# Kernel tuning notes

Measured on AMD Instinct MI355X. Metric: run time of the kernel, lower is better.

## Reference

```python
import jax, jax.numpy as jnp
import numpy as np

NEG_INF = jnp.finfo(jnp.float32).min

def setup_inputs() -> dict:
    key = jax.random.key(0)
    k1, k2, k3, k4 = jax.random.split(key, 4)
    B, H, S, DK, DV = 2, 16, 2048, 64, 64
    Q = jax.random.normal(k1, (B, H, S, DK), dtype=jnp.float32)
    K = jax.random.normal(k2, (B, H, S, DK), dtype=jnp.float32)
    V = jax.random.normal(k3, (B, H, S, DV), dtype=jnp.float32)
    mask = jax.random.randint(k4, (B, 1, S, S), 0, 2, dtype=jnp.int32)
    return {"Q": Q, "K": K, "V": V, "mask": mask}

def reference(Q, K, V, mask):
    d_k = Q.shape[-1]
    # scores: [B, H, Sq, Sk]
    scores = jnp.einsum('bhqd,bhkd->bhqk', Q, K) / jnp.sqrt(jnp.float32(d_k))
    scores = jnp.where(mask == 0, NEG_INF, scores)
    attn_weights = jax.nn.softmax(scores, axis=-1)
    # dropout p=0.0 -> identity (eval-mode reference)
    output = jnp.einsum('bhqk,bhkv->bhqv', attn_weights, V)
    return (output, attn_weights)
```

## Files before the change

kernel.cpp:

```cpp
#include <hip/hip_runtime.h>


typedef __attribute__((ext_vector_type(4))) float f32x4;
typedef __attribute__((ext_vector_type(8))) short s16x8;
typedef __attribute__((ext_vector_type(4))) unsigned short u16x4;
typedef __attribute__((ext_vector_type(8))) unsigned short u16x8;
typedef __attribute__((ext_vector_type(4))) unsigned int u32x4;

#define S_LEN 2048
#define D_DIM 64
#define H_NUM 16
#define B_NUM 2
#define NT    32
#define SW    32
#define QSCALE 0.18033688011112042f

__device__ __forceinline__ int swz(int row, int colByte) {
  return row * 128 + (colByte ^ ((row & 7) << 4));
}

__device__ __forceinline__ unsigned short f2bf(float f) {
  unsigned int x = __builtin_bit_cast(unsigned int, f);
  x = (x + 0x7FFFu + ((x >> 16) & 1u)) >> 16;
  return (unsigned short)x;
}

__device__ __forceinline__ unsigned cvt_pk_bf16(float lo, float hi) {
  unsigned r;
  asm("v_cvt_pk_bf16_f32 %0, %1, %2" : "=v"(r) : "v"(lo), "v"(hi));
  return r;
}

__device__ __forceinline__ f32x4 mfma16(f32x4 acc, s16x8 a, s16x8 b) {
  return __builtin_amdgcn_mfma_f32_16x16x32_bf16(a, b, acc, 0, 0, 0);
}


__global__ __launch_bounds__(256) void prep_kernel(
    const float* __restrict__ Q, const float* __restrict__ K,
    const float* __restrict__ V, const int* __restrict__ m,
    u16x4* __restrict__ Q16, u16x4* __restrict__ K16,
    unsigned short* __restrict__ VT, unsigned long long* __restrict__ bits)
{
  const int blk = blockIdx.x;
  const int tid = threadIdx.x;

  if (blk < 1024) {
    __shared__ unsigned short t[64][72];
    const int bh = blk >> 5;
    const int st = blk & 31;
    const float* src = V + ((size_t)bh * S_LEN + st * 64) * D_DIM;
    const int r0 = tid >> 4;
    const int c  = (tid & 15) * 4;
#pragma unroll
    for (int i = 0; i < 4; ++i) {
      const int r = r0 + i * 16;
      float4 v = *(const float4*)(src + r * D_DIM + c);
      t[c + 0][r] = f2bf(v.x); t[c + 1][r] = f2bf(v.y);
      t[c + 2][r] = f2bf(v.z); t[c + 3][r] = f2bf(v.w);
    }
    __syncthreads();
#pragma unroll
    for (int i = 0; i < 4; ++i) {
      const int idx = tid + i * 256;
      const int d  = idx >> 4;
      const int t0 = (idx & 15) * 4;
      const int sp = ((t0 >> 5) & 1) * 32 + ((t0 & 7) >> 2) * 16 + ((t0 >> 3) & 3) * 4;
      u16x4 o = *(const u16x4*)&t[d][sp];
      *(u16x4*)(VT + ((size_t)bh * D_DIM + d) * S_LEN + st * 64 + t0) = o;
    }
  } else if (blk < 2048) {
    const int n4 = B_NUM * H_NUM * S_LEN * D_DIM / 4;
    const int step = 1024 * 256;
    for (int i = (blk - 1024) * 256 + tid; i < n4; i += step) {
      float4 q = ((const float4*)Q)[i];
      Q16[i] = u16x4{f2bf(q.x * QSCALE), f2bf(q.y * QSCALE),
                     f2bf(q.z * QSCALE), f2bf(q.w * QSCALE)};
      float4 k = ((const float4*)K)[i];
      K16[i] = u16x4{f2bf(k.x), f2bf(k.y), f2bf(k.z), f2bf(k.w)};
    }
  } else {
    const int total = B_NUM * S_LEN * S_LEN;
    const int step  = 1024 * 256;
    for (int i = (blk - 2048) * 256 + tid; i < total; i += step) {
      unsigned long long b = __ballot(m[i] != 0);
      if ((tid & 63) == 0) bits[i >> 6] = b;
    }
  }
}


__global__ __launch_bounds__(256) void attn_fused_kernel(
    const unsigned short* __restrict__ Q16, const unsigned short* __restrict__ K16,
    const unsigned short* __restrict__ VT16, const unsigned long long* __restrict__ Mb,
    float* __restrict__ Op, float* __restrict__ Wp)
{
  const int tid  = threadIdx.x;
  const int lane = tid & 63;
  const int wv   = tid >> 6;
  const int l15  = lane & 15;
  const int g4   = lane >> 4;

  const int wg = blockIdx.x;
  const int lg = (wg & 7) * 128 + (wg >> 3);
  const int qt = lg & 31;
  const int bh = lg >> 5;
  const int b  = bh >> 4;

  __shared__ __align__(16) char lds[32768];
  char* Kbuf = lds;
  char* Vbuf = lds + 16384;

  const unsigned short* Qg16 = Q16 + ((size_t)bh * S_LEN + qt * 64 + wv * 16 + l15) * D_DIM + g4 * 8;
  const unsigned short* Kg16 = K16 + (size_t)bh * S_LEN * D_DIM;
  const unsigned short* Vg   = VT16 + (size_t)bh * D_DIM * S_LEN;
  float* Og = Op + ((size_t)bh * S_LEN + qt * 64) * D_DIM;
  float* Wg = Wp + ((size_t)bh * S_LEN + qt * 64) * S_LEN;
  const unsigned long long* Mg = Mb + ((size_t)b * S_LEN + qt * 64) * SW;

  const s16x8 qa0 = *(const s16x8*)Qg16;
  const s16x8 qa1 = *(const s16x8*)(Qg16 + 32);

  f32x4 oacc[4];
#pragma unroll
  for (int i = 0; i < 4; ++i) oacc[i] = f32x4{0.f, 0.f, 0.f, 0.f};
  float lps = 0.f;

  const int sr  = tid >> 3;
  const int ss  = tid & 7;
  const int ssb = ss * 16;

  {
    u16x8 k0 = *(const u16x8*)(Kg16 + (size_t)sr * D_DIM + ss * 8);
    u16x8 k1 = *(const u16x8*)(Kg16 + (size_t)(sr + 32) * D_DIM + ss * 8);
    u16x8 v0 = *(const u16x8*)(Vg + (size_t)sr * S_LEN + ss * 8);
    u16x8 v1 = *(const u16x8*)(Vg + (size_t)(sr + 32) * S_LEN + ss * 8);
    *(u16x8*)(Kbuf + swz(sr, ssb))      = k0;
    *(u16x8*)(Kbuf + swz(sr + 32, ssb)) = k1;
    *(u16x8*)(Vbuf + swz(sr, ssb))      = v0;
    *(u16x8*)(Vbuf + swz(sr + 32, ssb)) = v1;
  }
  __syncthreads();

  int cur = 0;
  for (int kt = 0; kt < NT; ++kt) {
    const int ktn = (kt + 1 < NT) ? kt + 1 : kt;
    u16x8 kr0 = *(const u16x8*)(Kg16 + (size_t)(ktn * 64 + sr) * D_DIM + ss * 8);
    u16x8 kr1 = *(const u16x8*)(Kg16 + (size_t)(ktn * 64 + sr + 32) * D_DIM + ss * 8);
    u16x8 vr0 = *(const u16x8*)(Vg + (size_t)sr * S_LEN + ktn * 64 + ss * 8);
    u16x8 vr1 = *(const u16x8*)(Vg + (size_t)(sr + 32) * S_LEN + ktn * 64 + ss * 8);
    __builtin_amdgcn_sched_barrier(0);

    char* Kc = Kbuf + cur * 8192;
    char* Vc = Vbuf + cur * 8192;

    const unsigned long long mw = Mg[(wv * 16 + l15) * SW + kt];

    f32x4 sacc[4];
#pragma unroll
    for (int i = 0; i < 4; ++i) sacc[i] = f32x4{0.f, 0.f, 0.f, 0.f};
#pragma unroll
    for (int ct = 0; ct < 4; ++ct) {
      s16x8 b0 = *(const s16x8*)(Kc + swz(ct * 16 + l15, g4 * 16));
      s16x8 b1 = *(const s16x8*)(Kc + swz(ct * 16 + l15, g4 * 16 + 64));
      sacc[ct] = mfma16(sacc[ct], b0, qa0);
      sacc[ct] = mfma16(sacc[ct], b1, qa1);
    }

    float ev[4][4];
#pragma unroll
    for (int ct = 0; ct < 4; ++ct) {
#pragma unroll
      for (int r = 0; r < 4; ++r) {
        float e = __builtin_amdgcn_exp2f(sacc[ct][r]);
        e = ((mw >> (ct * 16 + g4 * 4 + r)) & 1ull) ? e : 0.f;
        ev[ct][r] = e;
      }
      lps += (ev[ct][0] + ev[ct][1]) + (ev[ct][2] + ev[ct][3]);
    }
    const u32x4 a0 = {cvt_pk_bf16(ev[0][0], ev[0][1]), cvt_pk_bf16(ev[0][2], ev[0][3]),
                      cvt_pk_bf16(ev[1][0], ev[1][1]), cvt_pk_bf16(ev[1][2], ev[1][3])};
    const u32x4 a1 = {cvt_pk_bf16(ev[2][0], ev[2][1]), cvt_pk_bf16(ev[2][2], ev[2][3]),
                      cvt_pk_bf16(ev[3][0], ev[3][1]), cvt_pk_bf16(ev[3][2], ev[3][3])};
    const s16x8 pa0 = __builtin_bit_cast(s16x8, a0);
    const s16x8 pa1 = __builtin_bit_cast(s16x8, a1);

#pragma unroll
    for (int ct = 0; ct < 4; ++ct) {
      s16x8 v0 = *(const s16x8*)(Vc + swz(ct * 16 + l15, g4 * 16));
      s16x8 v1 = *(const s16x8*)(Vc + swz(ct * 16 + l15, g4 * 16 + 64));
      oacc[ct] = mfma16(oacc[ct], pa0, v0);
      oacc[ct] = mfma16(oacc[ct], pa1, v1);
    }

    char* Kn = Kbuf + (cur ^ 1) * 8192;
    char* Vn = Vbuf + (cur ^ 1) * 8192;
    *(u16x8*)(Kn + swz(sr, ssb))      = kr0;
    *(u16x8*)(Kn + swz(sr + 32, ssb)) = kr1;
    *(u16x8*)(Vn + swz(sr, ssb))      = vr0;
    *(u16x8*)(Vn + swz(sr + 32, ssb)) = vr1;
    __syncthreads();
    cur ^= 1;
  }

  lps += __shfl_xor(lps, 16);
  lps += __shfl_xor(lps, 32);
  const float lpr = 1.0f / lps;

  float lpn[4];
#pragma unroll
  for (int r = 0; r < 4; ++r) lpn[r] = __shfl(lpr, g4 * 4 + r);

#pragma unroll
  for (int ct = 0; ct < 4; ++ct)
#pragma unroll
    for (int r = 0; r < 4; ++r)
      Og[(size_t)(wv * 16 + g4 * 4 + r) * D_DIM + ct * 16 + l15] = oacc[ct][r] * lpn[r];

  __builtin_amdgcn_sched_barrier(0);

  float* Wrow = Wg + (size_t)(wv * 16 + l15) * S_LEN;
  const unsigned long long* Mrow = Mg + (wv * 16 + l15) * SW;

  s16x8 kb0[4], kb1[4];
#pragma unroll
  for (int ct = 0; ct < 4; ++ct) {
    const unsigned short* kp = Kg16 + (size_t)(ct * 16 + l15) * D_DIM + g4 * 8;
    kb0[ct] = *(const s16x8*)kp;
    kb1[ct] = *(const s16x8*)(kp + 32);
  }

  for (int kt = 0; kt < NT; ++kt) {
    const int ktn = (kt < NT - 1) ? kt + 1 : kt;
    s16x8 nk0[4], nk1[4];
#pragma unroll
    for (int ct = 0; ct < 4; ++ct) {
      const unsigned short* kp = Kg16 + (size_t)(ktn * 64 + ct * 16 + l15) * D_DIM + g4 * 8;
      nk0[ct] = *(const s16x8*)kp;
      nk1[ct] = *(const s16x8*)(kp + 32);
    }

    const unsigned long long mw = Mrow[kt];

    f32x4 sacc[4];
#pragma unroll
    for (int i = 0; i < 4; ++i) sacc[i] = f32x4{0.f, 0.f, 0.f, 0.f};
#pragma unroll
    for (int ct = 0; ct < 4; ++ct) {
      sacc[ct] = mfma16(sacc[ct], kb0[ct], qa0);
      sacc[ct] = mfma16(sacc[ct], kb1[ct], qa1);
    }

#pragma unroll
    for (int ct = 0; ct < 4; ++ct) {
      f32x4 w;
#pragma unroll
      for (int r = 0; r < 4; ++r) {
        float e = __builtin_amdgcn_exp2f(sacc[ct][r]);
        w[r] = ((mw >> (ct * 16 + g4 * 4 + r)) & 1ull) ? e * lpr : 0.f;
      }
      __builtin_nontemporal_store(w,
          (f32x4*)(Wrow + (size_t)kt * 64 + ct * 16 + g4 * 4));
    }
#pragma unroll
    for (int ct = 0; ct < 4; ++ct) { kb0[ct] = nk0[ct]; kb1[ct] = nk1[ct]; }
  }
}


__global__ __launch_bounds__(256) void attn_fwd_kernel(
    const float* __restrict__ Qp, const float* __restrict__ Kp, const float* __restrict__ Vp,
    const int* __restrict__ Mi, float* __restrict__ Op, float* __restrict__ Wp)
{
  const int tid  = threadIdx.x;
  const int lane = tid & 63;
  const int wv   = tid >> 6;
  const int l15  = lane & 15;
  const int g4   = lane >> 4;

  const int wg = blockIdx.x;
  const int lg = (wg & 7) * 128 + (wg >> 3);
  const int qt = lg & 31;
  const int bh = lg >> 5;
  const int b  = bh >> 4;

  __shared__ __align__(16) char lds[32768];
  char* Qs  = lds;
  char* Ks  = lds + 8192;
  char* VTs = lds + 16384;
  char* Ps  = lds + 24576 + (wv << 11);

  const float* Qg = Qp + ((size_t)bh * S_LEN + qt * 64) * D_DIM;
  const float* Kg = Kp + (size_t)bh * S_LEN * D_DIM;
  const float* Vg = Vp + (size_t)bh * S_LEN * D_DIM;
  float* Og = Op + ((size_t)bh * S_LEN + qt * 64) * D_DIM;
  float* Wg = Wp + ((size_t)bh * S_LEN + qt * 64) * S_LEN;
  const int* Mig = Mi + ((size_t)b * S_LEN + qt * 64) * S_LEN;

  {
    const int r0 = tid >> 4;
    const int c  = (tid & 15) * 4;
#pragma unroll
    for (int i = 0; i < 4; ++i) {
      const int r = r0 + i * 16;
      float4 v = *(const float4*)(Qg + r * D_DIM + c);
      ushort4 p; p.x = f2bf(v.x); p.y = f2bf(v.y); p.z = f2bf(v.z); p.w = f2bf(v.w);
      *(ushort4*)(Qs + swz(r, c * 2)) = p;
    }
  }
  __syncthreads();
  const s16x8 qa0 = *(const s16x8*)(Qs + swz(wv * 16 + l15, g4 * 16));
  const s16x8 qa1 = *(const s16x8*)(Qs + swz(wv * 16 + l15, g4 * 16 + 64));

  f32x4 oacc[4];
#pragma unroll
  for (int i = 0; i < 4; ++i) oacc[i] = f32x4{0.f, 0.f, 0.f, 0.f};
  float lp[4] = {0.f, 0.f, 0.f, 0.f};

  const int qrow = wv * 16 + g4 * 4;

  for (int kt = 0; kt < NT; ++kt) {
    __syncthreads();
    {
      const int r0 = tid >> 4;
      const int c  = (tid & 15) * 4;
      const float* Kt = Kg + kt * 64 * D_DIM;
#pragma unroll
      for (int i = 0; i < 4; ++i) {
        const int r = r0 + i * 16;
        float4 v = *(const float4*)(Kt + r * D_DIM + c);
        ushort4 p; p.x = f2bf(v.x); p.y = f2bf(v.y); p.z = f2bf(v.z); p.w = f2bf(v.w);
        *(ushort4*)(Ks + swz(r, c * 2)) = p;
      }
      const float* Vt = Vg + kt * 64 * D_DIM;
#pragma unroll
      for (int i = 0; i < 2; ++i) {
        const int rr = (tid >> 4) * 2 + i * 32;
        float4 a  = *(const float4*)(Vt + rr * D_DIM + c);
        float4 bq = *(const float4*)(Vt + (rr + 1) * D_DIM + c);
        const float av[4] = {a.x, a.y, a.z, a.w};
        const float bv[4] = {bq.x, bq.y, bq.z, bq.w};
#pragma unroll
        for (int j = 0; j < 4; ++j) {
          unsigned pk = (unsigned)f2bf(av[j]) | ((unsigned)f2bf(bv[j]) << 16);
          *(unsigned*)(VTs + swz(c + j, rr * 2)) = pk;
        }
      }
    }
    __syncthreads();

    f32x4 sacc[4];
#pragma unroll
    for (int i = 0; i < 4; ++i) sacc[i] = f32x4{0.f, 0.f, 0.f, 0.f};
#pragma unroll
    for (int ct = 0; ct < 4; ++ct) {
      s16x8 b0 = *(const s16x8*)(Ks + swz(ct * 16 + l15, g4 * 16));
      s16x8 b1 = *(const s16x8*)(Ks + swz(ct * 16 + l15, g4 * 16 + 64));
      sacc[ct] = mfma16(sacc[ct], qa0, b0);
      sacc[ct] = mfma16(sacc[ct], qa1, b1);
    }

#pragma unroll
    for (int ct = 0; ct < 4; ++ct) {
#pragma unroll
      for (int r = 0; r < 4; ++r) {
        float e = __expf(sacc[ct][r] * 0.125f);
        bool keep = Mig[(size_t)(qrow + r) * S_LEN + kt * 64 + ct * 16 + l15] != 0;
        e = keep ? e : 0.f;
        lp[r] += e;
        *(unsigned short*)(Ps + swz(g4 * 4 + r, (ct * 16 + l15) * 2)) = f2bf(e);
      }
    }
    asm volatile("s_waitcnt lgkmcnt(0)" ::: "memory");
    __builtin_amdgcn_sched_barrier(0);

    const s16x8 pa0 = *(const s16x8*)(Ps + swz(l15, g4 * 16));
    const s16x8 pa1 = *(const s16x8*)(Ps + swz(l15, g4 * 16 + 64));
#pragma unroll
    for (int ct = 0; ct < 4; ++ct) {
      s16x8 v0 = *(const s16x8*)(VTs + swz(ct * 16 + l15, g4 * 16));
      s16x8 v1 = *(const s16x8*)(VTs + swz(ct * 16 + l15, g4 * 16 + 64));
      oacc[ct] = mfma16(oacc[ct], pa0, v0);
      oacc[ct] = mfma16(oacc[ct], pa1, v1);
    }
  }

#pragma unroll
  for (int r = 0; r < 4; ++r) {
    float v = lp[r];
    v += __shfl_xor(v, 1);
    v += __shfl_xor(v, 2);
    v += __shfl_xor(v, 4);
    v += __shfl_xor(v, 8);
    lp[r] = 1.0f / v;
  }

#pragma unroll
  for (int ct = 0; ct < 4; ++ct)
#pragma unroll
    for (int r = 0; r < 4; ++r)
      Og[(size_t)(qrow + r) * D_DIM + ct * 16 + l15] = oacc[ct][r] * lp[r];

  for (int kt = 0; kt < NT; ++kt) {
    __syncthreads();
    {
      const int r0 = tid >> 4;
      const int c  = (tid & 15) * 4;
      const float* Kt = Kg + kt * 64 * D_DIM;
#pragma unroll
      for (int i = 0; i < 4; ++i) {
        const int r = r0 + i * 16;
        float4 v = *(const float4*)(Kt + r * D_DIM + c);
        ushort4 p; p.x = f2bf(v.x); p.y = f2bf(v.y); p.z = f2bf(v.z); p.w = f2bf(v.w);
        *(ushort4*)(Ks + swz(r, c * 2)) = p;
      }
    }
    __syncthreads();

    f32x4 sacc[4];
#pragma unroll
    for (int i = 0; i < 4; ++i) sacc[i] = f32x4{0.f, 0.f, 0.f, 0.f};
#pragma unroll
    for (int ct = 0; ct < 4; ++ct) {
      s16x8 b0 = *(const s16x8*)(Ks + swz(ct * 16 + l15, g4 * 16));
      s16x8 b1 = *(const s16x8*)(Ks + swz(ct * 16 + l15, g4 * 16 + 64));
      sacc[ct] = mfma16(sacc[ct], qa0, b0);
      sacc[ct] = mfma16(sacc[ct], qa1, b1);
    }

#pragma unroll
    for (int ct = 0; ct < 4; ++ct) {
#pragma unroll
      for (int r = 0; r < 4; ++r) {
        float e = __expf(sacc[ct][r] * 0.125f);
        bool keep = Mig[(size_t)(qrow + r) * S_LEN + kt * 64 + ct * 16 + l15] != 0;
        e = keep ? e : 0.f;
        __builtin_nontemporal_store(e * lp[r],
            Wg + (size_t)(qrow + r) * S_LEN + kt * 64 + ct * 16 + l15);
      }
    }
  }
}

extern "C" void kernel_launch(void* const* d_in, const int* in_sizes, int n_in,
                              void* d_out, int out_size, void* d_ws, size_t ws_size,
                              hipStream_t stream) {
  (void)in_sizes; (void)n_in; (void)out_size;
  const float* Q   = (const float*)d_in[0];
  const float* K   = (const float*)d_in[1];
  const float* V   = (const float*)d_in[2];
  const int* mask  = (const int*)d_in[3];
  float* Out = (float*)d_out;
  float* W   = Out + (size_t)B_NUM * H_NUM * S_LEN * D_DIM;

  const size_t bits_bytes = (size_t)(B_NUM * S_LEN * S_LEN / 64) * 8;
  const size_t t16_bytes  = (size_t)B_NUM * H_NUM * S_LEN * D_DIM * 2;
  unsigned long long* bits = (unsigned long long*)d_ws;

  if (ws_size >= bits_bytes + 3 * t16_bytes) {
    unsigned short* Q16 = (unsigned short*)((char*)d_ws + bits_bytes);
    unsigned short* K16 = Q16 + t16_bytes / 2;
    unsigned short* VT  = K16 + t16_bytes / 2;
    prep_kernel<<<3072, 256, 0, stream>>>(Q, K, V, mask,
                                          (u16x4*)Q16, (u16x4*)K16, VT, bits);
    attn_fused_kernel<<<1024, 256, 0, stream>>>(Q16, K16, VT, bits, Out, W);
  } else {
    attn_fwd_kernel<<<1024, 256, 0, stream>>>(Q, K, V, mask, Out, W);
  }
}
```

Before: 239.9 us.

## Share K/V LDS tiles across two query tiles with 512-thread blocks

```diff
diff --git a/kernel.cpp b/kernel.cpp
--- a/kernel.cpp
+++ b/kernel.cpp
@@ -90,7 +90,7 @@
 }
 
 
-__global__ __launch_bounds__(256) void attn_fused_kernel(
+__global__ __launch_bounds__(512, 4) void attn_fused_kernel(
     const unsigned short* __restrict__ Q16, const unsigned short* __restrict__ K16,
     const unsigned short* __restrict__ VT16, const unsigned long long* __restrict__ Mb,
     float* __restrict__ Op, float* __restrict__ Wp)
@@ -100,18 +100,20 @@
   const int wv   = tid >> 6;
   const int l15  = lane & 15;
   const int g4   = lane >> 4;
+  const int wt   = wv & 3;
 
   const int wg = blockIdx.x;
-  const int lg = (wg & 7) * 128 + (wg >> 3);
-  const int qt = lg & 31;
-  const int bh = lg >> 5;
+  const int lg = (wg & 7) * 64 + (wg >> 3);
+  const int tp = lg & 15;
+  const int bh = lg >> 4;
   const int b  = bh >> 4;
+  const int qt = tp * 2 + (wv >> 2);
 
   __shared__ __align__(16) char lds[32768];
   char* Kbuf = lds;
   char* Vbuf = lds + 16384;
 
-  const unsigned short* Qg16 = Q16 + ((size_t)bh * S_LEN + qt * 64 + wv * 16 + l15) * D_DIM + g4 * 8;
+  const unsigned short* Qg16 = Q16 + ((size_t)bh * S_LEN + qt * 64 + wt * 16 + l15) * D_DIM + g4 * 8;
   const unsigned short* Kg16 = K16 + (size_t)bh * S_LEN * D_DIM;
   const unsigned short* Vg   = VT16 + (size_t)bh * D_DIM * S_LEN;
   float* Og = Op + ((size_t)bh * S_LEN + qt * 64) * D_DIM;
@@ -132,29 +134,23 @@
 
   {
     u16x8 k0 = *(const u16x8*)(Kg16 + (size_t)sr * D_DIM + ss * 8);
-    u16x8 k1 = *(const u16x8*)(Kg16 + (size_t)(sr + 32) * D_DIM + ss * 8);
     u16x8 v0 = *(const u16x8*)(Vg + (size_t)sr * S_LEN + ss * 8);
-    u16x8 v1 = *(const u16x8*)(Vg + (size_t)(sr + 32) * S_LEN + ss * 8);
-    *(u16x8*)(Kbuf + swz(sr, ssb))      = k0;
-    *(u16x8*)(Kbuf + swz(sr + 32, ssb)) = k1;
-    *(u16x8*)(Vbuf + swz(sr, ssb))      = v0;
-    *(u16x8*)(Vbuf + swz(sr + 32, ssb)) = v1;
+    *(u16x8*)(Kbuf + swz(sr, ssb)) = k0;
+    *(u16x8*)(Vbuf + swz(sr, ssb)) = v0;
   }
   __syncthreads();
 
   int cur = 0;
   for (int kt = 0; kt < NT; ++kt) {
     const int ktn = (kt + 1 < NT) ? kt + 1 : kt;
-    u16x8 kr0 = *(const u16x8*)(Kg16 + (size_t)(ktn * 64 + sr) * D_DIM + ss * 8);
-    u16x8 kr1 = *(const u16x8*)(Kg16 + (size_t)(ktn * 64 + sr + 32) * D_DIM + ss * 8);
-    u16x8 vr0 = *(const u16x8*)(Vg + (size_t)sr * S_LEN + ktn * 64 + ss * 8);
-    u16x8 vr1 = *(const u16x8*)(Vg + (size_t)(sr + 32) * S_LEN + ktn * 64 + ss * 8);
+    u16x8 kr = *(const u16x8*)(Kg16 + (size_t)(ktn * 64 + sr) * D_DIM + ss * 8);
+    u16x8 vr = *(const u16x8*)(Vg + (size_t)sr * S_LEN + ktn * 64 + ss * 8);
     __builtin_amdgcn_sched_barrier(0);
 
     char* Kc = Kbuf + cur * 8192;
     char* Vc = Vbuf + cur * 8192;
 
-    const unsigned long long mw = Mg[(wv * 16 + l15) * SW + kt];
+    const unsigned long long mw = Mg[(wt * 16 + l15) * SW + kt];
 
     f32x4 sacc[4];
 #pragma unroll
@@ -167,23 +163,23 @@
       sacc[ct] = mfma16(sacc[ct], b1, qa1);
     }
 
-    float ev[4][4];
-#pragma unroll
-    for (int ct = 0; ct < 4; ++ct) {
-#pragma unroll
-      for (int r = 0; r < 4; ++r) {
-        float e = __builtin_amdgcn_exp2f(sacc[ct][r]);
-        e = ((mw >> (ct * 16 + g4 * 4 + r)) & 1ull) ? e : 0.f;
-        ev[ct][r] = e;
-      }
-      lps += (ev[ct][0] + ev[ct][1]) + (ev[ct][2] + ev[ct][3]);
-    }
-    const u32x4 a0 = {cvt_pk_bf16(ev[0][0], ev[0][1]), cvt_pk_bf16(ev[0][2], ev[0][3]),
-                      cvt_pk_bf16(ev[1][0], ev[1][1]), cvt_pk_bf16(ev[1][2], ev[1][3])};
-    const u32x4 a1 = {cvt_pk_bf16(ev[2][0], ev[2][1]), cvt_pk_bf16(ev[2][2], ev[2][3]),
-                      cvt_pk_bf16(ev[3][0], ev[3][1]), cvt_pk_bf16(ev[3][2], ev[3][3])};
-    const s16x8 pa0 = __builtin_bit_cast(s16x8, a0);
-    const s16x8 pa1 = __builtin_bit_cast(s16x8, a1);
+    unsigned pw[8];
+#pragma unroll
+    for (int ct = 0; ct < 4; ++ct) {
+      float e0 = __builtin_amdgcn_exp2f(sacc[ct][0]);
+      float e1 = __builtin_amdgcn_exp2f(sacc[ct][1]);
+      float e2 = __builtin_amdgcn_exp2f(sacc[ct][2]);
+      float e3 = __builtin_amdgcn_exp2f(sacc[ct][3]);
+      e0 = ((mw >> (ct * 16 + g4 * 4 + 0)) & 1ull) ? e0 : 0.f;
+      e1 = ((mw >> (ct * 16 + g4 * 4 + 1)) & 1ull) ? e1 : 0.f;
+      e2 = ((mw >> (ct * 16 + g4 * 4 + 2)) & 1ull) ? e2 : 0.f;
+      e3 = ((mw >> (ct * 16 + g4 * 4 + 3)) & 1ull) ? e3 : 0.f;
+      lps += (e0 + e1) + (e2 + e3);
+      pw[2 * ct]     = cvt_pk_bf16(e0, e1);
+      pw[2 * ct + 1] = cvt_pk_bf16(e2, e3);
+    }
+    const s16x8 pa0 = __builtin_bit_cast(s16x8, u32x4{pw[0], pw[1], pw[2], pw[3]});
+    const s16x8 pa1 = __builtin_bit_cast(s16x8, u32x4{pw[4], pw[5], pw[6], pw[7]});
 
 #pragma unroll
     for (int ct = 0; ct < 4; ++ct) {
@@ -195,10 +191,8 @@
 
     char* Kn = Kbuf + (cur ^ 1) * 8192;
     char* Vn = Vbuf + (cur ^ 1) * 8192;
-    *(u16x8*)(Kn + swz(sr, ssb))      = kr0;
-    *(u16x8*)(Kn + swz(sr + 32, ssb)) = kr1;
-    *(u16x8*)(Vn + swz(sr, ssb))      = vr0;
-    *(u16x8*)(Vn + swz(sr + 32, ssb)) = vr1;
+    *(u16x8*)(Kn + swz(sr, ssb)) = kr;
+    *(u16x8*)(Vn + swz(sr, ssb)) = vr;
     __syncthreads();
     cur ^= 1;
   }
@@ -215,12 +209,12 @@
   for (int ct = 0; ct < 4; ++ct)
 #pragma unroll
     for (int r = 0; r < 4; ++r)
-      Og[(size_t)(wv * 16 + g4 * 4 + r) * D_DIM + ct * 16 + l15] = oacc[ct][r] * lpn[r];
+      Og[(size_t)(wt * 16 + g4 * 4 + r) * D_DIM + ct * 16 + l15] = oacc[ct][r] * lpn[r];
 
   __builtin_amdgcn_sched_barrier(0);
 
-  float* Wrow = Wg + (size_t)(wv * 16 + l15) * S_LEN;
-  const unsigned long long* Mrow = Mg + (wv * 16 + l15) * SW;
+  float* Wrow = Wg + (size_t)(wt * 16 + l15) * S_LEN;
+  const unsigned long long* Mrow = Mg + (wt * 16 + l15) * SW;
 
   s16x8 kb0[4], kb1[4];
 #pragma unroll
@@ -463,7 +457,7 @@
     unsigned short* VT  = K16 + t16_bytes / 2;
     prep_kernel<<<3072, 256, 0, stream>>>(Q, K, V, mask,
                                           (u16x4*)Q16, (u16x4*)K16, VT, bits);
-    attn_fused_kernel<<<1024, 256, 0, stream>>>(Q16, K16, VT, bits, Out, W);
+    attn_fused_kernel<<<512, 512, 0, stream>>>(Q16, K16, VT, bits, Out, W);
   } else {
     attn_fwd_kernel<<<1024, 256, 0, stream>>>(Q, K, V, mask, Out, W);
   }
```

Measured after the change: 230.1 us. 1.04x faster.

## Split attention into row-sum pass and fused PV plus weights-write pass

Applied to the files above, without the earlier changes.

```diff
diff --git a/kernel.cpp b/kernel.cpp
--- a/kernel.cpp
+++ b/kernel.cpp
@@ -90,10 +90,9 @@
 }
 
 
-__global__ __launch_bounds__(256) void attn_fused_kernel(
+__global__ __launch_bounds__(256) void attn_rowsum_kernel(
     const unsigned short* __restrict__ Q16, const unsigned short* __restrict__ K16,
-    const unsigned short* __restrict__ VT16, const unsigned long long* __restrict__ Mb,
-    float* __restrict__ Op, float* __restrict__ Wp)
+    const unsigned long long* __restrict__ Mb, float* __restrict__ lpq)
 {
   const int tid  = threadIdx.x;
   const int lane = tid & 63;
@@ -107,6 +106,90 @@
   const int bh = lg >> 5;
   const int b  = bh >> 4;
 
+  __shared__ __align__(16) char Kbuf[16384];
+
+  const unsigned short* Qg16 = Q16 + ((size_t)bh * S_LEN + qt * 64 + wv * 16 + l15) * D_DIM + g4 * 8;
+  const unsigned short* Kg16 = K16 + (size_t)bh * S_LEN * D_DIM;
+  float* lpg = lpq + (size_t)bh * S_LEN + qt * 64;
+  const unsigned long long* Mg = Mb + ((size_t)b * S_LEN + qt * 64) * SW;
+
+  const s16x8 qa0 = *(const s16x8*)Qg16;
+  const s16x8 qa1 = *(const s16x8*)(Qg16 + 32);
+
+  float lps = 0.f;
+
+  const int sr  = tid >> 3;
+  const int ss  = tid & 7;
+  const int ssb = ss * 16;
+
+  {
+    u16x8 k0 = *(const u16x8*)(Kg16 + (size_t)sr * D_DIM + ss * 8);
+    u16x8 k1 = *(const u16x8*)(Kg16 + (size_t)(sr + 32) * D_DIM + ss * 8);
+    *(u16x8*)(Kbuf + swz(sr, ssb))      = k0;
+    *(u16x8*)(Kbuf + swz(sr + 32, ssb)) = k1;
+  }
+  __syncthreads();
+
+  int cur = 0;
+  for (int kt = 0; kt < NT; ++kt) {
+    const int ktn = (kt + 1 < NT) ? kt + 1 : kt;
+    u16x8 kr0 = *(const u16x8*)(Kg16 + (size_t)(ktn * 64 + sr) * D_DIM + ss * 8);
+    u16x8 kr1 = *(const u16x8*)(Kg16 + (size_t)(ktn * 64 + sr + 32) * D_DIM + ss * 8);
+    __builtin_amdgcn_sched_barrier(0);
+
+    char* Kc = Kbuf + cur * 8192;
+    const unsigned long long mw = Mg[(wv * 16 + l15) * SW + kt];
+
+    f32x4 sacc[4];
+#pragma unroll
+    for (int i = 0; i < 4; ++i) sacc[i] = f32x4{0.f, 0.f, 0.f, 0.f};
+#pragma unroll
+    for (int ct = 0; ct < 4; ++ct) {
+      s16x8 b0 = *(const s16x8*)(Kc + swz(ct * 16 + l15, g4 * 16));
+      s16x8 b1 = *(const s16x8*)(Kc + swz(ct * 16 + l15, g4 * 16 + 64));
+      sacc[ct] = mfma16(sacc[ct], b0, qa0);
+      sacc[ct] = mfma16(sacc[ct], b1, qa1);
+    }
+
+#pragma unroll
+    for (int ct = 0; ct < 4; ++ct) {
+#pragma unroll
+      for (int r = 0; r < 4; ++r) {
+        float e = __builtin_amdgcn_exp2f(sacc[ct][r]);
+        lps += ((mw >> (ct * 16 + g4 * 4 + r)) & 1ull) ? e : 0.f;
+      }
+    }
+
+    char* Kn = Kbuf + (cur ^ 1) * 8192;
+    *(u16x8*)(Kn + swz(sr, ssb))      = kr0;
+    *(u16x8*)(Kn + swz(sr + 32, ssb)) = kr1;
+    __syncthreads();
+    cur ^= 1;
+  }
+
+  lps += __shfl_xor(lps, 16);
+  lps += __shfl_xor(lps, 32);
+  if (g4 == 0) lpg[wv * 16 + l15] = 1.0f / lps;
+}
+
+
+__global__ __launch_bounds__(256) void attn_main_kernel(
+    const unsigned short* __restrict__ Q16, const unsigned short* __restrict__ K16,
+    const unsigned short* __restrict__ VT16, const unsigned long long* __restrict__ Mb,
+    const float* __restrict__ lpq, float* __restrict__ Op, float* __restrict__ Wp)
+{
+  const int tid  = threadIdx.x;
+  const int lane = tid & 63;
+  const int wv   = tid >> 6;
+  const int l15  = lane & 15;
+  const int g4   = lane >> 4;
+
+  const int wg = blockIdx.x;
+  const int lg = (wg & 7) * 128 + (wg >> 3);
+  const int qt = lg & 31;
+  const int bh = lg >> 5;
+  const int b  = bh >> 4;
+
   __shared__ __align__(16) char lds[32768];
   char* Kbuf = lds;
   char* Vbuf = lds + 16384;
@@ -115,16 +198,21 @@
   const unsigned short* Kg16 = K16 + (size_t)bh * S_LEN * D_DIM;
   const unsigned short* Vg   = VT16 + (size_t)bh * D_DIM * S_LEN;
   float* Og = Op + ((size_t)bh * S_LEN + qt * 64) * D_DIM;
-  float* Wg = Wp + ((size_t)bh * S_LEN + qt * 64) * S_LEN;
+  float* Wrow = Wp + ((size_t)bh * S_LEN + qt * 64 + wv * 16 + l15) * S_LEN;
   const unsigned long long* Mg = Mb + ((size_t)b * S_LEN + qt * 64) * SW;
+  const float* lpg = lpq + (size_t)bh * S_LEN + qt * 64;
 
   const s16x8 qa0 = *(const s16x8*)Qg16;
   const s16x8 qa1 = *(const s16x8*)(Qg16 + 32);
 
+  const float lpr = lpg[wv * 16 + l15];
+  float lpn[4];
+#pragma unroll
+  for (int r = 0; r < 4; ++r) lpn[r] = lpg[wv * 16 + g4 * 4 + r];
+
   f32x4 oacc[4];
 #pragma unroll
   for (int i = 0; i < 4; ++i) oacc[i] = f32x4{0.f, 0.f, 0.f, 0.f};
-  float lps = 0.f;
 
   const int sr  = tid >> 3;
   const int ss  = tid & 7;
@@ -167,23 +255,25 @@
       sacc[ct] = mfma16(sacc[ct], b1, qa1);
     }
 
-    float ev[4][4];
-#pragma unroll
-    for (int ct = 0; ct < 4; ++ct) {
-#pragma unroll
-      for (int r = 0; r < 4; ++r) {
-        float e = __builtin_amdgcn_exp2f(sacc[ct][r]);
-        e = ((mw >> (ct * 16 + g4 * 4 + r)) & 1ull) ? e : 0.f;
-        ev[ct][r] = e;
-      }
-      lps += (ev[ct][0] + ev[ct][1]) + (ev[ct][2] + ev[ct][3]);
-    }
-    const u32x4 a0 = {cvt_pk_bf16(ev[0][0], ev[0][1]), cvt_pk_bf16(ev[0][2], ev[0][3]),
-                      cvt_pk_bf16(ev[1][0], ev[1][1]), cvt_pk_bf16(ev[1][2], ev[1][3])};
-    const u32x4 a1 = {cvt_pk_bf16(ev[2][0], ev[2][1]), cvt_pk_bf16(ev[2][2], ev[2][3]),
-                      cvt_pk_bf16(ev[3][0], ev[3][1]), cvt_pk_bf16(ev[3][2], ev[3][3])};
-    const s16x8 pa0 = __builtin_bit_cast(s16x8, a0);
-    const s16x8 pa1 = __builtin_bit_cast(s16x8, a1);
+    unsigned pw[8];
+#pragma unroll
+    for (int ct = 0; ct < 4; ++ct) {
+      float e0 = __builtin_amdgcn_exp2f(sacc[ct][0]);
+      float e1 = __builtin_amdgcn_exp2f(sacc[ct][1]);
+      float e2 = __builtin_amdgcn_exp2f(sacc[ct][2]);
+      float e3 = __builtin_amdgcn_exp2f(sacc[ct][3]);
+      e0 = ((mw >> (ct * 16 + g4 * 4 + 0)) & 1ull) ? e0 : 0.f;
+      e1 = ((mw >> (ct * 16 + g4 * 4 + 1)) & 1ull) ? e1 : 0.f;
+      e2 = ((mw >> (ct * 16 + g4 * 4 + 2)) & 1ull) ? e2 : 0.f;
+      e3 = ((mw >> (ct * 16 + g4 * 4 + 3)) & 1ull) ? e3 : 0.f;
+      f32x4 w = {e0 * lpr, e1 * lpr, e2 * lpr, e3 * lpr};
+      __builtin_nontemporal_store(w,
+          (f32x4*)(Wrow + (size_t)kt * 64 + ct * 16 + g4 * 4));
+      pw[2 * ct]     = cvt_pk_bf16(e0, e1);
+      pw[2 * ct + 1] = cvt_pk_bf16(e2, e3);
+    }
+    const s16x8 pa0 = __builtin_bit_cast(s16x8, u32x4{pw[0], pw[1], pw[2], pw[3]});
+    const s16x8 pa1 = __builtin_bit_cast(s16x8, u32x4{pw[4], pw[5], pw[6], pw[7]});
 
 #pragma unroll
     for (int ct = 0; ct < 4; ++ct) {
@@ -203,68 +293,11 @@
     cur ^= 1;
   }
 
-  lps += __shfl_xor(lps, 16);
-  lps += __shfl_xor(lps, 32);
-  const float lpr = 1.0f / lps;
-
-  float lpn[4];
-#pragma unroll
-  for (int r = 0; r < 4; ++r) lpn[r] = __shfl(lpr, g4 * 4 + r);
-
 #pragma unroll
   for (int ct = 0; ct < 4; ++ct)
 #pragma unroll
     for (int r = 0; r < 4; ++r)
       Og[(size_t)(wv * 16 + g4 * 4 + r) * D_DIM + ct * 16 + l15] = oacc[ct][r] * lpn[r];
-
-  __builtin_amdgcn_sched_barrier(0);
-
-  float* Wrow = Wg + (size_t)(wv * 16 + l15) * S_LEN;
-  const unsigned long long* Mrow = Mg + (wv * 16 + l15) * SW;
-
-  s16x8 kb0[4], kb1[4];
-#pragma unroll
-  for (int ct = 0; ct < 4; ++ct) {
-    const unsigned short* kp = Kg16 + (size_t)(ct * 16 + l15) * D_DIM + g4 * 8;
-    kb0[ct] = *(const s16x8*)kp;
-    kb1[ct] = *(const s16x8*)(kp + 32);
-  }
-
-  for (int kt = 0; kt < NT; ++kt) {
-    const int ktn = (kt < NT - 1) ? kt + 1 : kt;
-    s16x8 nk0[4], nk1[4];
-#pragma unroll
-    for (int ct = 0; ct < 4; ++ct) {
-      const unsigned short* kp = Kg16 + (size_t)(ktn * 64 + ct * 16 + l15) * D_DIM + g4 * 8;
-      nk0[ct] = *(const s16x8*)kp;
-      nk1[ct] = *(const s16x8*)(kp + 32);
-    }
-
-    const unsigned long long mw = Mrow[kt];
-
-    f32x4 sacc[4];
-#pragma unroll
-    for (int i = 0; i < 4; ++i) sacc[i] = f32x4{0.f, 0.f, 0.f, 0.f};
-#pragma unroll
-    for (int ct = 0; ct < 4; ++ct) {
-      sacc[ct] = mfma16(sacc[ct], kb0[ct], qa0);
-      sacc[ct] = mfma16(sacc[ct], kb1[ct], qa1);
-    }
-
-#pragma unroll
-    for (int ct = 0; ct < 4; ++ct) {
-      f32x4 w;
-#pragma unroll
-      for (int r = 0; r < 4; ++r) {
-        float e = __builtin_amdgcn_exp2f(sacc[ct][r]);
-        w[r] = ((mw >> (ct * 16 + g4 * 4 + r)) & 1ull) ? e * lpr : 0.f;
-      }
-      __builtin_nontemporal_store(w,
-          (f32x4*)(Wrow + (size_t)kt * 64 + ct * 16 + g4 * 4));
-    }
-#pragma unroll
-    for (int ct = 0; ct < 4; ++ct) { kb0[ct] = nk0[ct]; kb1[ct] = nk1[ct]; }
-  }
 }
 
 
@@ -455,15 +488,18 @@
 
   const size_t bits_bytes = (size_t)(B_NUM * S_LEN * S_LEN / 64) * 8;
   const size_t t16_bytes  = (size_t)B_NUM * H_NUM * S_LEN * D_DIM * 2;
+  const size_t lp_bytes   = (size_t)B_NUM * H_NUM * S_LEN * 4;
   unsigned long long* bits = (unsigned long long*)d_ws;
 
-  if (ws_size >= bits_bytes + 3 * t16_bytes) {
+  if (ws_size >= bits_bytes + 3 * t16_bytes + lp_bytes) {
     unsigned short* Q16 = (unsigned short*)((char*)d_ws + bits_bytes);
     unsigned short* K16 = Q16 + t16_bytes / 2;
     unsigned short* VT  = K16 + t16_bytes / 2;
+    float* lpq = (float*)((char*)d_ws + bits_bytes + 3 * t16_bytes);
     prep_kernel<<<3072, 256, 0, stream>>>(Q, K, V, mask,
                                           (u16x4*)Q16, (u16x4*)K16, VT, bits);
-    attn_fused_kernel<<<1024, 256, 0, stream>>>(Q16, K16, VT, bits, Out, W);
+    attn_rowsum_kernel<<<1024, 256, 0, stream>>>(Q16, K16, bits, lpq);
+    attn_main_kernel<<<1024, 256, 0, stream>>>(Q16, K16, VT, bits, lpq, Out, W);
   } else {
     attn_fwd_kernel<<<1024, 256, 0, stream>>>(Q, K, V, mask, Out, W);
   }
```

Result: faster. 230.2 us (median of 3 runs) (-4.1%).

## Precompute softmax row sums in separate kernel and write weights during PV pass

Applied to the files above, without the earlier changes.

```diff
diff --git a/kernel.cpp b/kernel.cpp
--- a/kernel.cpp
+++ b/kernel.cpp
@@ -13,6 +13,7 @@
 #define B_NUM 2
 #define NT    32
 #define SW    32
+#define BHS   (B_NUM * H_NUM * S_LEN)
 #define QSCALE 0.18033688011112042f
 
 __device__ __forceinline__ int swz(int row, int colByte) {
@@ -90,10 +91,9 @@
 }
 
 
-__global__ __launch_bounds__(256) void attn_fused_kernel(
+__global__ __launch_bounds__(256) void attn_rowsum_kernel(
     const unsigned short* __restrict__ Q16, const unsigned short* __restrict__ K16,
-    const unsigned short* __restrict__ VT16, const unsigned long long* __restrict__ Mb,
-    float* __restrict__ Op, float* __restrict__ Wp)
+    const unsigned long long* __restrict__ Mb, float* __restrict__ lp2)
 {
   const int tid  = threadIdx.x;
   const int lane = tid & 63;
@@ -102,6 +102,85 @@
   const int g4   = lane >> 4;
 
   const int wg = blockIdx.x;
+  const int lg = (wg & 7) * 256 + (wg >> 3);
+  const int kc = lg & 1;
+  const int qt = (lg >> 1) & 31;
+  const int bh = lg >> 6;
+  const int b  = bh >> 4;
+
+  const int row = qt * 64 + wv * 16 + l15;
+
+  const unsigned short* Qg16 = Q16 + ((size_t)bh * S_LEN + row) * D_DIM + g4 * 8;
+  const unsigned short* Kg16 = K16 + (size_t)bh * S_LEN * D_DIM;
+  const unsigned long long* Mrow = Mb + ((size_t)b * S_LEN + row) * SW;
+
+  const s16x8 qa0 = *(const s16x8*)Qg16;
+  const s16x8 qa1 = *(const s16x8*)(Qg16 + 32);
+
+  float lps = 0.f;
+  const int kt0 = kc * (NT / 2);
+  const int kt1 = kt0 + (NT / 2);
+
+  s16x8 kb0[4], kb1[4];
+#pragma unroll
+  for (int ct = 0; ct < 4; ++ct) {
+    const unsigned short* kp = Kg16 + (size_t)(kt0 * 64 + ct * 16 + l15) * D_DIM + g4 * 8;
+    kb0[ct] = *(const s16x8*)kp;
+    kb1[ct] = *(const s16x8*)(kp + 32);
+  }
+  unsigned long long mw = Mrow[kt0];
+
+  for (int kt = kt0; kt < kt1; ++kt) {
+    const int ktn = (kt + 1 < kt1) ? kt + 1 : kt;
+    s16x8 nk0[4], nk1[4];
+#pragma unroll
+    for (int ct = 0; ct < 4; ++ct) {
+      const unsigned short* kp = Kg16 + (size_t)(ktn * 64 + ct * 16 + l15) * D_DIM + g4 * 8;
+      nk0[ct] = *(const s16x8*)kp;
+      nk1[ct] = *(const s16x8*)(kp + 32);
+    }
+    const unsigned long long mwn = Mrow[ktn];
+
+    f32x4 sacc[4];
+#pragma unroll
+    for (int i = 0; i < 4; ++i) sacc[i] = f32x4{0.f, 0.f, 0.f, 0.f};
+#pragma unroll
+    for (int ct = 0; ct < 4; ++ct) {
+      sacc[ct] = mfma16(sacc[ct], kb0[ct], qa0);
+      sacc[ct] = mfma16(sacc[ct], kb1[ct], qa1);
+    }
+
+#pragma unroll
+    for (int ct = 0; ct < 4; ++ct) {
+#pragma unroll
+      for (int r = 0; r < 4; ++r) {
+        float e = __builtin_amdgcn_exp2f(sacc[ct][r]);
+        lps += ((mw >> (ct * 16 + g4 * 4 + r)) & 1ull) ? e : 0.f;
+      }
+    }
+    mw = mwn;
+#pragma unroll
+    for (int ct = 0; ct < 4; ++ct) { kb0[ct] = nk0[ct]; kb1[ct] = nk1[ct]; }
+  }
+
+  lps += __shfl_xor(lps, 16);
+  lps += __shfl_xor(lps, 32);
+  if (g4 == 0) lp2[(size_t)kc * BHS + (size_t)bh * S_LEN + row] = lps;
+}
+
+
+__global__ __launch_bounds__(256) void attn_main_kernel(
+    const unsigned short* __restrict__ Q16, const unsigned short* __restrict__ K16,
+    const unsigned short* __restrict__ VT16, const unsigned long long* __restrict__ Mb,
+    const float* __restrict__ lp2, float* __restrict__ Op, float* __restrict__ Wp)
+{
+  const int tid  = threadIdx.x;
+  const int lane = tid & 63;
+  const int wv   = tid >> 6;
+  const int l15  = lane & 15;
+  const int g4   = lane >> 4;
+
+  const int wg = blockIdx.x;
   const int lg = (wg & 7) * 128 + (wg >> 3);
   const int qt = lg & 31;
   const int bh = lg >> 5;
@@ -115,16 +194,23 @@
   const unsigned short* Kg16 = K16 + (size_t)bh * S_LEN * D_DIM;
   const unsigned short* Vg   = VT16 + (size_t)bh * D_DIM * S_LEN;
   float* Og = Op + ((size_t)bh * S_LEN + qt * 64) * D_DIM;
-  float* Wg = Wp + ((size_t)bh * S_LEN + qt * 64) * S_LEN;
-  const unsigned long long* Mg = Mb + ((size_t)b * S_LEN + qt * 64) * SW;
+  float* Wrow = Wp + ((size_t)bh * S_LEN + qt * 64 + wv * 16 + l15) * S_LEN;
+  const unsigned long long* Mrow = Mb + ((size_t)b * S_LEN + qt * 64 + wv * 16 + l15) * SW;
+  const float* lpA = lp2 + (size_t)bh * S_LEN + qt * 64;
+  const float* lpB = lpA + BHS;
 
   const s16x8 qa0 = *(const s16x8*)Qg16;
   const s16x8 qa1 = *(const s16x8*)(Qg16 + 32);
 
+  const float lpr = 1.0f / (lpA[wv * 16 + l15] + lpB[wv * 16 + l15]);
+  float lpn[4];
+#pragma unroll
+  for (int r = 0; r < 4; ++r)
+    lpn[r] = 1.0f / (lpA[wv * 16 + g4 * 4 + r] + lpB[wv * 16 + g4 * 4 + r]);
+
   f32x4 oacc[4];
 #pragma unroll
   for (int i = 0; i < 4; ++i) oacc[i] = f32x4{0.f, 0.f, 0.f, 0.f};
-  float lps = 0.f;
 
   const int sr  = tid >> 3;
   const int ss  = tid & 7;
@@ -140,6 +226,7 @@
     *(u16x8*)(Vbuf + swz(sr, ssb))      = v0;
     *(u16x8*)(Vbuf + swz(sr + 32, ssb)) = v1;
   }
+  unsigned long long mw = Mrow[0];
   __syncthreads();
 
   int cur = 0;
@@ -149,12 +236,11 @@
     u16x8 kr1 = *(const u16x8*)(Kg16 + (size_t)(ktn * 64 + sr + 32) * D_DIM + ss * 8);
     u16x8 vr0 = *(const u16x8*)(Vg + (size_t)sr * S_LEN + ktn * 64 + ss * 8);
     u16x8 vr1 = *(const u16x8*)(Vg + (size_t)(sr + 32) * S_LEN + ktn * 64 + ss * 8);
+    const unsigned long long mwn = Mrow[ktn];
     __builtin_amdgcn_sched_barrier(0);
 
     char* Kc = Kbuf + cur * 8192;
     char* Vc = Vbuf + cur * 8192;
-
-    const unsigned long long mw = Mg[(wv * 16 + l15) * SW + kt];
 
     f32x4 sacc[4];
 #pragma unroll
@@ -167,23 +253,25 @@
       sacc[ct] = mfma16(sacc[ct], b1, qa1);
     }
 
-    float ev[4][4];
-#pragma unroll
-    for (int ct = 0; ct < 4; ++ct) {
-#pragma unroll
-      for (int r = 0; r < 4; ++r) {
-        float e = __builtin_amdgcn_exp2f(sacc[ct][r]);
-        e = ((mw >> (ct * 16 + g4 * 4 + r)) & 1ull) ? e : 0.f;
-        ev[ct][r] = e;
-      }
-      lps += (ev[ct][0] + ev[ct][1]) + (ev[ct][2] + ev[ct][3]);
-    }
-    const u32x4 a0 = {cvt_pk_bf16(ev[0][0], ev[0][1]), cvt_pk_bf16(ev[0][2], ev[0][3]),
-                      cvt_pk_bf16(ev[1][0], ev[1][1]), cvt_pk_bf16(ev[1][2], ev[1][3])};
-    const u32x4 a1 = {cvt_pk_bf16(ev[2][0], ev[2][1]), cvt_pk_bf16(ev[2][2], ev[2][3]),
-                      cvt_pk_bf16(ev[3][0], ev[3][1]), cvt_pk_bf16(ev[3][2], ev[3][3])};
-    const s16x8 pa0 = __builtin_bit_cast(s16x8, a0);
-    const s16x8 pa1 = __builtin_bit_cast(s16x8, a1);
+    unsigned pw[8];
+#pragma unroll
+    for (int ct = 0; ct < 4; ++ct) {
+      float e0 = __builtin_amdgcn_exp2f(sacc[ct][0]);
+      float e1 = __builtin_amdgcn_exp2f(sacc[ct][1]);
+      float e2 = __builtin_amdgcn_exp2f(sacc[ct][2]);
+      float e3 = __builtin_amdgcn_exp2f(sacc[ct][3]);
+      e0 = ((mw >> (ct * 16 + g4 * 4 + 0)) & 1ull) ? e0 : 0.f;
+      e1 = ((mw >> (ct * 16 + g4 * 4 + 1)) & 1ull) ? e1 : 0.f;
+      e2 = ((mw >> (ct * 16 + g4 * 4 + 2)) & 1ull) ? e2 : 0.f;
+      e3 = ((mw >> (ct * 16 + g4 * 4 + 3)) & 1ull) ? e3 : 0.f;
+      f32x4 w = {e0 * lpr, e1 * lpr, e2 * lpr, e3 * lpr};
+      __builtin_nontemporal_store(w,
+          (f32x4*)(Wrow + (size_t)kt * 64 + ct * 16 + g4 * 4));
+      pw[2 * ct]     = cvt_pk_bf16(e0, e1);
+      pw[2 * ct + 1] = cvt_pk_bf16(e2, e3);
+    }
+    const s16x8 pa0 = __builtin_bit_cast(s16x8, u32x4{pw[0], pw[1], pw[2], pw[3]});
+    const s16x8 pa1 = __builtin_bit_cast(s16x8, u32x4{pw[4], pw[5], pw[6], pw[7]});
 
 #pragma unroll
     for (int ct = 0; ct < 4; ++ct) {
@@ -199,72 +287,16 @@
     *(u16x8*)(Kn + swz(sr + 32, ssb)) = kr1;
     *(u16x8*)(Vn + swz(sr, ssb))      = vr0;
     *(u16x8*)(Vn + swz(sr + 32, ssb)) = vr1;
+    mw = mwn;
     __syncthreads();
     cur ^= 1;
   }
 
-  lps += __shfl_xor(lps, 16);
-  lps += __shfl_xor(lps, 32);
-  const float lpr = 1.0f / lps;
-
-  float lpn[4];
-#pragma unroll
-  for (int r = 0; r < 4; ++r) lpn[r] = __shfl(lpr, g4 * 4 + r);
-
 #pragma unroll
   for (int ct = 0; ct < 4; ++ct)
 #pragma unroll
     for (int r = 0; r < 4; ++r)
       Og[(size_t)(wv * 16 + g4 * 4 + r) * D_DIM + ct * 16 + l15] = oacc[ct][r] * lpn[r];
-
-  __builtin_amdgcn_sched_barrier(0);
-
-  float* Wrow = Wg + (size_t)(wv * 16 + l15) * S_LEN;
-  const unsigned long long* Mrow = Mg + (wv * 16 + l15) * SW;
-
-  s16x8 kb0[4], kb1[4];
-#pragma unroll
-  for (int ct = 0; ct < 4; ++ct) {
-    const unsigned short* kp = Kg16 + (size_t)(ct * 16 + l15) * D_DIM + g4 * 8;
-    kb0[ct] = *(const s16x8*)kp;
-    kb1[ct] = *(const s16x8*)(kp + 32);
-  }
-
-  for (int kt = 0; kt < NT; ++kt) {
-    const int ktn = (kt < NT - 1) ? kt + 1 : kt;
-    s16x8 nk0[4], nk1[4];
-#pragma unroll
-    for (int ct = 0; ct < 4; ++ct) {
-      const unsigned short* kp = Kg16 + (size_t)(ktn * 64 + ct * 16 + l15) * D_DIM + g4 * 8;
-      nk0[ct] = *(const s16x8*)kp;
-      nk1[ct] = *(const s16x8*)(kp + 32);
-    }
-
-    const unsigned long long mw = Mrow[kt];
-
-    f32x4 sacc[4];
-#pragma unroll
-    for (int i = 0; i < 4; ++i) sacc[i] = f32x4{0.f, 0.f, 0.f, 0.f};
-#pragma unroll
-    for (int ct = 0; ct < 4; ++ct) {
-      sacc[ct] = mfma16(sacc[ct], kb0[ct], qa0);
-      sacc[ct] = mfma16(sacc[ct], kb1[ct], qa1);
-    }
-
-#pragma unroll
-    for (int ct = 0; ct < 4; ++ct) {
-      f32x4 w;
-#pragma unroll
-      for (int r = 0; r < 4; ++r) {
-        float e = __builtin_amdgcn_exp2f(sacc[ct][r]);
-        w[r] = ((mw >> (ct * 16 + g4 * 4 + r)) & 1ull) ? e * lpr : 0.f;
-      }
-      __builtin_nontemporal_store(w,
-          (f32x4*)(Wrow + (size_t)kt * 64 + ct * 16 + g4 * 4));
-    }
-#pragma unroll
-    for (int ct = 0; ct < 4; ++ct) { kb0[ct] = nk0[ct]; kb1[ct] = nk1[ct]; }
-  }
 }
 
 
@@ -455,15 +487,18 @@
 
   const size_t bits_bytes = (size_t)(B_NUM * S_LEN * S_LEN / 64) * 8;
   const size_t t16_bytes  = (size_t)B_NUM * H_NUM * S_LEN * D_DIM * 2;
+  const size_t lp2_bytes  = (size_t)2 * BHS * 4;
   unsigned long long* bits = (unsigned long long*)d_ws;
 
-  if (ws_size >= bits_bytes + 3 * t16_bytes) {
+  if (ws_size >= bits_bytes + 3 * t16_bytes + lp2_bytes) {
     unsigned short* Q16 = (unsigned short*)((char*)d_ws + bits_bytes);
     unsigned short* K16 = Q16 + t16_bytes / 2;
     unsigned short* VT  = K16 + t16_bytes / 2;
+    float* lp2 = (float*)((char*)d_ws + bits_bytes + 3 * t16_bytes);
     prep_kernel<<<3072, 256, 0, stream>>>(Q, K, V, mask,
                                           (u16x4*)Q16, (u16x4*)K16, VT, bits);
-    attn_fused_kernel<<<1024, 256, 0, stream>>>(Q16, K16, VT, bits, Out, W);
+    attn_rowsum_kernel<<<2048, 256, 0, stream>>>(Q16, K16, bits, lp2);
+    attn_main_kernel<<<1024, 256, 0, stream>>>(Q16, K16, VT, bits, lp2, Out, W);
   } else {
     attn_fwd_kernel<<<1024, 256, 0, stream>>>(Q, K, V, mask, Out, W);
   }
```

After: 323.5 us. 1.35x slower.
